# Optimization experiments

Measured on AMD Instinct MI355X. Metric: run time of the kernel, lower is better.

The kernel has to match this reference:

```python
import jax, jax.numpy as jnp
import numpy as np

NUM_WINDOWS = 162   # icosphere order-2 windows
NUM_HEADS = 8

def layernorm(x, g, b, eps=1e-5):
    m = jnp.mean(x, axis=-1, keepdims=True)
    v = jnp.var(x, axis=-1, keepdims=True)
    return (x - m) * jax.lax.rsqrt(v + eps) * g + b

def setup_inputs() -> dict:
    key = jax.random.key(0)
    ks = jax.random.split(key, 16)
    B, N, C = 1, 41472, 512
    H, hid = NUM_HEADS, 4 * 512
    s = 0.02
    # window assignment: 162 windows x 256 vertices, shuffled (gather-based partition)
    rng = np.random.default_rng(0)
    wid = np.repeat(np.arange(NUM_WINDOWS), N // NUM_WINDOWS)
    rng.shuffle(wid)
    return {
        "x": jax.random.normal(ks[0], (B, N, C), jnp.float32),
        "mesh": jax.random.normal(ks[1], (N, 3), jnp.float32),
        "ln1_g": jnp.ones((C,), jnp.float32),
        "ln1_b": jnp.zeros((C,), jnp.float32),
        "qkv_w": jax.random.normal(ks[2], (C, 3 * C), jnp.float32) * s,
        "qkv_b": jnp.zeros((3 * C,), jnp.float32),
        "rel_bias": jax.random.normal(ks[3], (H, 1, 1), jnp.float32) * s,
        "proj_w": jax.random.normal(ks[4], (C, C), jnp.float32) * s,
        "proj_b": jnp.zeros((C,), jnp.float32),
        "ln2_g": jnp.ones((C,), jnp.float32),
        "ln2_b": jnp.zeros((C,), jnp.float32),
        "ffn_w1": jax.random.normal(ks[5], (C, hid), jnp.float32) * s,
        "ffn_b1": jnp.zeros((hid,), jnp.float32),
        "ffn_w2": jax.random.normal(ks[6], (hid, C), jnp.float32) * s,
        "ffn_b2": jnp.zeros((C,), jnp.float32),
        "window_ids": jnp.asarray(wid, dtype=jnp.int32),
    }

def reference(x, mesh, ln1_g, ln1_b, qkv_w, qkv_b, rel_bias, proj_w, proj_b,
              ln2_g, ln2_b, ffn_w1, ffn_b1, ffn_w2, ffn_b2, window_ids):
    B, N, C = x.shape
    H = NUM_HEADS
    hd = C // H
    ws = N // NUM_WINDOWS
    # --- gather-based window partition ---
    idx = jnp.argsort(window_ids)                      # [N]
    w = x[:, idx, :].reshape(B * NUM_WINDOWS, ws, C)   # [BW, ws, C]
    # --- window attention on norm1(windows) ---
    h = layernorm(w, ln1_g, ln1_b)
    qkv = (h @ qkv_w + qkv_b).reshape(B * NUM_WINDOWS, ws, 3, H, hd)
    q, k, v = qkv[:, :, 0], qkv[:, :, 1], qkv[:, :, 2]  # [BW, ws, H, hd]
    scale = hd ** -0.5
    attn = jnp.einsum('wqhd,wkhd->whqk', q, k) * scale + rel_bias
    attn = jax.nn.softmax(attn, axis=-1)
    out = jnp.einsum('whqk,wkhd->wqhd', attn, v).reshape(B * NUM_WINDOWS, ws, C)
    out = out @ proj_w + proj_b
    # --- reverse partition + residual ---
    inv = jnp.argsort(idx)
    x = x + out.reshape(B, N, C)[:, inv, :]
    # --- FFN block ---
    h2 = layernorm(x, ln2_g, ln2_b)
    f = jax.nn.gelu(h2 @ ffn_w1 + ffn_b1, approximate=False) @ ffn_w2 + ffn_b2
    x = x + f
    return (x, mesh)
```

## Files before the change

kernel.cpp:

```cpp
#include <hip/hip_runtime.h>
#include <hip/hip_bf16.h>
#include <math.h>

#define NW   162
#define WS   256
#define NH   8
#define HD   64
#define CC   512
#define NTOK 41472
#define HID  2048

typedef __bf16 bf16x8 __attribute__((ext_vector_type(8)));
typedef float  floatx4 __attribute__((ext_vector_type(4)));

__device__ __forceinline__ void gload_lds16(const __bf16* g, __bf16* l) {
    __builtin_amdgcn_global_load_lds((const __attribute__((address_space(1))) void*)g,
                                     (__attribute__((address_space(3))) void*)l,
                                     16, 0, 0);
}

__global__ __launch_bounds__(256)
void build_perm_atomic(const int* __restrict__ wid, int* __restrict__ perm,
                       int* __restrict__ pos, int* __restrict__ counters) {
    const int i = blockIdx.x * 256 + threadIdx.x;
    const int w = wid[i];
    const int r = atomicAdd(&counters[w], 1);
    perm[w * WS + r] = i;
    pos[i] = w * WS + r;
}

__global__ void transpose_bf16(const float* __restrict__ in,
                               __bf16* __restrict__ out, int K, int N) {
    int idx = blockIdx.x * 256 + threadIdx.x;
    if (idx >= K * N) return;
    int n = idx / K, k = idx - n * K;
    out[idx] = (__bf16)in[(size_t)k * N + n];
}

__global__ __launch_bounds__(64)
void ln1_gather(const float* __restrict__ x, const int* __restrict__ perm,
                const float* __restrict__ g, const float* __restrict__ b,
                __bf16* __restrict__ h) {
    const int j = blockIdx.x, lane = threadIdx.x;
    const int orig = perm[j];
    const float4* xp = (const float4*)(x + (size_t)orig * CC);
    float4 a0 = xp[lane * 2 + 0], a1 = xp[lane * 2 + 1];
    float s  = a0.x + a0.y + a0.z + a0.w + a1.x + a1.y + a1.z + a1.w;
    float sq = a0.x*a0.x + a0.y*a0.y + a0.z*a0.z + a0.w*a0.w
             + a1.x*a1.x + a1.y*a1.y + a1.z*a1.z + a1.w*a1.w;
#pragma unroll
    for (int o = 32; o; o >>= 1) { s += __shfl_xor(s, o); sq += __shfl_xor(sq, o); }
    const float m  = s * (1.f / CC);
    const float rs = rsqrtf(sq * (1.f / CC) - m * m + 1e-5f);
    const float4* g4 = (const float4*)g;  const float4* b4 = (const float4*)b;
    float4 g0 = g4[lane*2+0], g1 = g4[lane*2+1], bb0 = b4[lane*2+0], bb1 = b4[lane*2+1];
    bf16x8 o8;
    o8[0] = (__bf16)((a0.x - m) * rs * g0.x + bb0.x);
    o8[1] = (__bf16)((a0.y - m) * rs * g0.y + bb0.y);
    o8[2] = (__bf16)((a0.z - m) * rs * g0.z + bb0.z);
    o8[3] = (__bf16)((a0.w - m) * rs * g0.w + bb0.w);
    o8[4] = (__bf16)((a1.x - m) * rs * g1.x + bb1.x);
    o8[5] = (__bf16)((a1.y - m) * rs * g1.y + bb1.y);
    o8[6] = (__bf16)((a1.z - m) * rs * g1.z + bb1.z);
    o8[7] = (__bf16)((a1.w - m) * rs * g1.w + bb1.w);
    *(bf16x8*)(h + (size_t)j * CC + lane * 8) = o8;
}

__global__ __launch_bounds__(64)
void resid_ln2(const float* __restrict__ x, const float* __restrict__ ptmp,
               const int* __restrict__ pos, const float* __restrict__ g,
               const float* __restrict__ b, float* __restrict__ xout,
               __bf16* __restrict__ h2) {
    const int i = blockIdx.x, lane = threadIdx.x;
    const int p = pos[i];
    const float4* xp = (const float4*)(x + (size_t)i * CC);
    const float4* pp = (const float4*)(ptmp + (size_t)p * CC);
    float4 a0 = xp[lane*2+0], a1 = xp[lane*2+1];
    float4 t0 = pp[lane*2+0], t1 = pp[lane*2+1];
    a0.x += t0.x; a0.y += t0.y; a0.z += t0.z; a0.w += t0.w;
    a1.x += t1.x; a1.y += t1.y; a1.z += t1.z; a1.w += t1.w;
    float4* op = (float4*)(xout + (size_t)i * CC);
    op[lane*2+0] = a0; op[lane*2+1] = a1;
    float s  = a0.x + a0.y + a0.z + a0.w + a1.x + a1.y + a1.z + a1.w;
    float sq = a0.x*a0.x + a0.y*a0.y + a0.z*a0.z + a0.w*a0.w
             + a1.x*a1.x + a1.y*a1.y + a1.z*a1.z + a1.w*a1.w;
#pragma unroll
    for (int o = 32; o; o >>= 1) { s += __shfl_xor(s, o); sq += __shfl_xor(sq, o); }
    const float m  = s * (1.f / CC);
    const float rs = rsqrtf(sq * (1.f / CC) - m * m + 1e-5f);
    const float4* g4 = (const float4*)g;  const float4* b4 = (const float4*)b;
    float4 g0 = g4[lane*2+0], g1 = g4[lane*2+1], bb0 = b4[lane*2+0], bb1 = b4[lane*2+1];
    bf16x8 o8;
    o8[0] = (__bf16)((a0.x - m) * rs * g0.x + bb0.x);
    o8[1] = (__bf16)((a0.y - m) * rs * g0.y + bb0.y);
    o8[2] = (__bf16)((a0.z - m) * rs * g0.z + bb0.z);
    o8[3] = (__bf16)((a0.w - m) * rs * g0.w + bb0.w);
    o8[4] = (__bf16)((a1.x - m) * rs * g1.x + bb1.x);
    o8[5] = (__bf16)((a1.y - m) * rs * g1.y + bb1.y);
    o8[6] = (__bf16)((a1.z - m) * rs * g1.z + bb1.z);
    o8[7] = (__bf16)((a1.w - m) * rs * g1.w + bb1.w);
    *(bf16x8*)(h2 + (size_t)i * CC + lane * 8) = o8;
}

template <int EPI>
__global__ __launch_bounds__(256)
void gemm_bt(const __bf16* __restrict__ A, const __bf16* __restrict__ Bt,
             const float* __restrict__ bias, const float* __restrict__ res,
             float* __restrict__ Cf, __bf16* __restrict__ Cb,
             int M, int N, int K) {
    __shared__ __bf16 As[128 * 64];
    __shared__ __bf16 Bs[128 * 64];
    const int tid = threadIdx.x;
    const int wave = tid >> 6, lane = tid & 63;
    const int wm = wave & 1, wn = wave >> 1;
    const int bm = blockIdx.y, bn = blockIdx.x;
    const int lr = lane & 15, lq = lane >> 4;

    floatx4 acc[4][4];
#pragma unroll
    for (int i = 0; i < 4; i++)
#pragma unroll
        for (int j = 0; j < 4; j++) acc[i][j] = (floatx4){0.f, 0.f, 0.f, 0.f};

    const int srow = tid >> 3;
    const int sseg = (tid & 7) ^ (srow & 7);
    const __bf16* gA = A  + (size_t)(bm * 128 + srow) * K + sseg * 8;
    const __bf16* gB = Bt + (size_t)(bn * 128 + srow) * K + sseg * 8;
    __bf16* lA = As + (size_t)(wave * 64) * 8;
    __bf16* lB = Bs + (size_t)(wave * 64) * 8;

    for (int kt = 0; kt < K; kt += 64) {
        __syncthreads();
#pragma unroll
        for (int j = 0; j < 4; j++) {
            gload_lds16(gA + (size_t)(j * 32) * K + kt, lA + j * 2048);
            gload_lds16(gB + (size_t)(j * 32) * K + kt, lB + j * 2048);
        }
        __syncthreads();
#pragma unroll
        for (int kk = 0; kk < 2; kk++) {
            bf16x8 af[4], bfr[4];
#pragma unroll
            for (int mt = 0; mt < 4; mt++)
                af[mt] = *(const bf16x8*)(As + (wm * 64 + mt * 16 + lr) * 64 +
                                          (((kk * 4 + lq) ^ (lr & 7)) * 8));
#pragma unroll
            for (int nt = 0; nt < 4; nt++)
                bfr[nt] = *(const bf16x8*)(Bs + (wn * 64 + nt * 16 + lr) * 64 +
                                           (((kk * 4 + lq) ^ (lr & 7)) * 8));
#pragma unroll
            for (int mt = 0; mt < 4; mt++)
#pragma unroll
                for (int nt = 0; nt < 4; nt++)
                    acc[mt][nt] = __builtin_amdgcn_mfma_f32_16x16x32_bf16(
                        af[mt], bfr[nt], acc[mt][nt], 0, 0, 0);
        }
    }

    if constexpr (EPI == 0 || EPI == 2) {
        __syncthreads();
        __bf16* rb = wm ? Bs : As;
#pragma unroll
        for (int mt = 0; mt < 4; mt++)
#pragma unroll
            for (int nt = 0; nt < 4; nt++) {
                const int cl = wn * 64 + nt * 16 + lr;
                const float bv = bias[bn * 128 + cl];
#pragma unroll
                for (int r = 0; r < 4; r++) {
                    float v = acc[mt][nt][r] + bv;
                    if constexpr (EPI == 2) {
                        const float u = 0.79788456080286535588f * (v + 0.044715f * v * v * v);
                        const float t = 1.f - 2.f / (1.f + __expf(2.f * u));
                        v = 0.5f * v * (1.f + t);
                    }
                    rb[(mt * 16 + lq * 4 + r) * 128 + cl] = (__bf16)v;
                }
            }
        __syncthreads();
#pragma unroll
        for (int j = 0; j < 8; j++) {
            const int c = j * 256 + tid;
            const __bf16* reg = (j < 4) ? As : Bs;
            const int rc = c & 1023;
            const int row = rc >> 4, seg = rc & 15;
            bf16x8 val = *(const bf16x8*)(reg + row * 128 + seg * 8);
            *(bf16x8*)(Cb + (size_t)(bm * 128 + (j >> 2) * 64 + row) * N +
                       bn * 128 + seg * 8) = val;
        }
    } else {
#pragma unroll
        for (int mt = 0; mt < 4; mt++) {
            const int row = bm * 128 + wm * 64 + mt * 16 + lq * 4;
#pragma unroll
            for (int nt = 0; nt < 4; nt++) {
                const int col = bn * 128 + wn * 64 + nt * 16 + lr;
                const float bv = bias[col];
#pragma unroll
                for (int r = 0; r < 4; r++) {
                    float v = acc[mt][nt][r] + bv;
                    const size_t off = (size_t)(row + r) * N + col;
                    if constexpr (EPI == 1) Cf[off] = v;
                    else                    Cf[off] = res[off] + v;
                }
            }
        }
    }
}

__global__ __launch_bounds__(256)
void attn_mfma(const __bf16* __restrict__ qkv, __bf16* __restrict__ aout,
               const float* __restrict__ rel_bias) {
    __shared__ __bf16 vs[WS][66];
    __shared__ __bf16 pbuf[4][64][34];
    const int w = blockIdx.x, h = blockIdx.y;
    const int tid = threadIdx.x;
    const int wave = tid >> 6, lane = tid & 63;
    const int lr = lane & 15, lq = lane >> 4;
    const size_t base = (size_t)w * (WS * 1536) + h * 64;

    for (int c = tid; c < WS * 8; c += 256) {
        const int key = c >> 3, d8 = c & 7;
        *(bf16x8*)(&vs[key][d8 * 8]) =
            *(const bf16x8*)(qkv + base + 1024 + (size_t)key * 1536 + d8 * 8);
    }

    const int q0 = wave * 64;
    bf16x8 qf[4][2];
#pragma unroll
    for (int mt = 0; mt < 4; mt++)
#pragma unroll
        for (int kk = 0; kk < 2; kk++)
            qf[mt][kk] = *(const bf16x8*)(qkv + base +
                (size_t)(q0 + mt * 16 + lr) * 1536 + kk * 32 + lq * 8);

    __syncthreads();

    floatx4 o[4][4];
    float lsum[4][4];
#pragma unroll
    for (int mt = 0; mt < 4; mt++)
#pragma unroll
        for (int dt = 0; dt < 4; dt++) o[mt][dt] = (floatx4){0.f, 0.f, 0.f, 0.f};
#pragma unroll
    for (int mt = 0; mt < 4; mt++)
#pragma unroll
        for (int r = 0; r < 4; r++) lsum[mt][r] = 0.f;

    const float sc = 0.125f * 1.44269504089f;
    const float bb = rel_bias[h] * 1.44269504089f;

    for (int kt = 0; kt < 8; kt++) {
        const int kbase = kt * 32;
        floatx4 s[4][2];
#pragma unroll
        for (int mt = 0; mt < 4; mt++)
#pragma unroll
            for (int nt = 0; nt < 2; nt++) s[mt][nt] = (floatx4){0.f, 0.f, 0.f, 0.f};
#pragma unroll
        for (int nt = 0; nt < 2; nt++) {
            const __bf16* kp = qkv + base + 512 + (size_t)(kbase + nt * 16 + lr) * 1536 + lq * 8;
            bf16x8 kf0 = *(const bf16x8*)(kp);
            bf16x8 kf1 = *(const bf16x8*)(kp + 32);
#pragma unroll
            for (int mt = 0; mt < 4; mt++) {
                s[mt][nt] = __builtin_amdgcn_mfma_f32_16x16x32_bf16(qf[mt][0], kf0, s[mt][nt], 0, 0, 0);
                s[mt][nt] = __builtin_amdgcn_mfma_f32_16x16x32_bf16(qf[mt][1], kf1, s[mt][nt], 0, 0, 0);
            }
        }
#pragma unroll
        for (int mt = 0; mt < 4; mt++)
#pragma unroll
            for (int nt = 0; nt < 2; nt++)
#pragma unroll
                for (int r = 0; r < 4; r++) {
                    float e = exp2f(s[mt][nt][r] * sc + bb);
                    lsum[mt][r] += e;
                    pbuf[wave][mt * 16 + lq * 4 + r][nt * 16 + lr] = (__bf16)e;
                }
        __syncthreads();
        bf16x8 vf[4];
#pragma unroll
        for (int dt = 0; dt < 4; dt++)
#pragma unroll
            for (int j = 0; j < 8; j++)
                vf[dt][j] = vs[kbase + lq * 8 + j][dt * 16 + lr];
#pragma unroll
        for (int mt = 0; mt < 4; mt++) {
            bf16x8 pf = *(const bf16x8*)(&pbuf[wave][mt * 16 + lr][lq * 8]);
#pragma unroll
            for (int dt = 0; dt < 4; dt++)
                o[mt][dt] = __builtin_amdgcn_mfma_f32_16x16x32_bf16(pf, vf[dt], o[mt][dt], 0, 0, 0);
        }
        __syncthreads();
    }

#pragma unroll
    for (int mt = 0; mt < 4; mt++)
#pragma unroll
        for (int r = 0; r < 4; r++) {
            float v = lsum[mt][r];
            v += __shfl_xor(v, 1); v += __shfl_xor(v, 2);
            v += __shfl_xor(v, 4); v += __shfl_xor(v, 8);
            lsum[mt][r] = 1.f / v;
        }

#pragma unroll
    for (int dh = 0; dh < 2; dh++) {
#pragma unroll
        for (int mt = 0; mt < 4; mt++)
#pragma unroll
            for (int dt = 0; dt < 2; dt++)
#pragma unroll
                for (int r = 0; r < 4; r++)
                    pbuf[wave][mt * 16 + lq * 4 + r][dt * 16 + lr] =
                        (__bf16)(o[mt][dh * 2 + dt][r] * lsum[mt][r]);
        __syncthreads();
#pragma unroll
        for (int it = 0; it < 4; it++) {
            const int c = it * 64 + lane;
            const int row = c >> 2, seg = c & 3;
            bf16x8 val = *(const bf16x8*)(&pbuf[wave][row][seg * 8]);
            *(bf16x8*)(aout + (size_t)(w * WS + q0 + row) * CC + h * 64 + dh * 32 + seg * 8) = val;
        }
        __syncthreads();
    }
}

extern "C" void kernel_launch(void* const* d_in, const int* in_sizes, int n_in,
                              void* d_out, int out_size, void* d_ws, size_t ws_size,
                              hipStream_t stream) {
    const float* x      = (const float*)d_in[0];
    const float* mesh   = (const float*)d_in[1];
    const float* ln1_g  = (const float*)d_in[2];
    const float* ln1_b  = (const float*)d_in[3];
    const float* qkv_w  = (const float*)d_in[4];
    const float* qkv_b  = (const float*)d_in[5];
    const float* rel_b  = (const float*)d_in[6];
    const float* proj_w = (const float*)d_in[7];
    const float* proj_b = (const float*)d_in[8];
    const float* ln2_g  = (const float*)d_in[9];
    const float* ln2_b  = (const float*)d_in[10];
    const float* w1     = (const float*)d_in[11];
    const float* b1     = (const float*)d_in[12];
    const float* w2     = (const float*)d_in[13];
    const float* b2     = (const float*)d_in[14];
    const int*   wid    = (const int*)d_in[15];

    char* ws = (char*)d_ws;
    int*    perm  = (int*)(ws + 0);
    int*    pos   = (int*)(ws + 165888);
    __bf16* wqkv  = (__bf16*)(ws + 331776);
    __bf16* wproj = (__bf16*)(ws + 1904640);
    __bf16* w1t   = (__bf16*)(ws + 2428928);
    __bf16* w2t   = (__bf16*)(ws + 4526080);
    const size_t BB = 6623232;
    __bf16* hln1 = (__bf16*)(ws + BB);
    __bf16* qkv  = (__bf16*)(ws + BB + 42467328);
    __bf16* aout = (__bf16*)(ws + BB + 169869312);
    float*  ptmp = (float*)(ws + BB);
    __bf16* h2   = (__bf16*)(ws + BB + 84934656);
    __bf16* f1   = (__bf16*)(ws + BB + 127401984);
    float*  xout = (float*)d_out;
    int*    counters = (int*)aout;

    hipMemsetAsync(counters, 0, NW * sizeof(int), stream);
    build_perm_atomic<<<NTOK / 256, 256, 0, stream>>>(wid, perm, pos, counters);

    transpose_bf16<<<(512 * 1536 + 255) / 256, 256, 0, stream>>>(qkv_w, wqkv, 512, 1536);
    transpose_bf16<<<(512 * 512 + 255) / 256, 256, 0, stream>>>(proj_w, wproj, 512, 512);
    transpose_bf16<<<(512 * 2048 + 255) / 256, 256, 0, stream>>>(w1, w1t, 512, 2048);
    transpose_bf16<<<(2048 * 512 + 255) / 256, 256, 0, stream>>>(w2, w2t, 2048, 512);

    ln1_gather<<<NTOK, 64, 0, stream>>>(x, perm, ln1_g, ln1_b, hln1);

    gemm_bt<0><<<dim3(1536 / 128, NTOK / 128), 256, 0, stream>>>(
        hln1, wqkv, qkv_b, nullptr, nullptr, qkv, NTOK, 1536, 512);

    attn_mfma<<<dim3(NW, NH), 256, 0, stream>>>(qkv, aout, rel_b);

    gemm_bt<1><<<dim3(512 / 128, NTOK / 128), 256, 0, stream>>>(
        aout, wproj, proj_b, nullptr, ptmp, nullptr, NTOK, 512, 512);

    resid_ln2<<<NTOK, 64, 0, stream>>>(x, ptmp, pos, ln2_g, ln2_b, xout, h2);

    gemm_bt<2><<<dim3(2048 / 128, NTOK / 128), 256, 0, stream>>>(
        h2, w1t, b1, nullptr, nullptr, f1, NTOK, 2048, 512);

    gemm_bt<3><<<dim3(512 / 128, NTOK / 128), 256, 0, stream>>>(
        f1, w2t, b2, xout, xout, nullptr, NTOK, 512, 2048);

    hipMemcpyAsync((char*)d_out + (size_t)NTOK * CC * 4, mesh,
                   (size_t)NTOK * 3 * 4, hipMemcpyDeviceToDevice, stream);
}
```

Baseline: 834.5 us.

## Swizzle transposed V in LDS, prefetch K, drop barriers, cheaper GELU

In the window attention kernel, V is now stored in LDS transposed with an XOR swizzle, so each lane fetches its MFMA B-fragment with one 16-byte load instead of eight scalar reads. K fragments for the next tile are loaded into registers one step ahead. Block-wide barriers around the per-wave P buffer are removed, since each wave only touches its own slice. The FFN GELU epilogue changes from the tanh form to x*sigmoid(1.702x) with a hardware reciprocal, and the softmax normalisation uses the same fast reciprocal. The sigmoid form and the fast reciprocal add numerical error relative to the exact-erf reference.

Measured after the change: 795.8 us. 4.6% less time.

```diff
diff --git a/kernel.cpp b/kernel.cpp
--- a/kernel.cpp
+++ b/kernel.cpp
@@ -18,6 +18,7 @@
                                      (__attribute__((address_space(3))) void*)l,
                                      16, 0, 0);
 }
+__device__ __forceinline__ float fast_rcp(float x) { return __builtin_amdgcn_rcpf(x); }
 
 __global__ __launch_bounds__(256)
 void build_perm_atomic(const int* __restrict__ wid, int* __restrict__ perm,
@@ -170,9 +171,8 @@
                 for (int r = 0; r < 4; r++) {
                     float v = acc[mt][nt][r] + bv;
                     if constexpr (EPI == 2) {
-                        const float u = 0.79788456080286535588f * (v + 0.044715f * v * v * v);
-                        const float t = 1.f - 2.f / (1.f + __expf(2.f * u));
-                        v = 0.5f * v * (1.f + t);
+                        const float e = __expf(v * -1.702f);
+                        v = v * fast_rcp(1.f + e);
                     }
                     rb[(mt * 16 + lq * 4 + r) * 128 + cl] = (__bf16)v;
                 }
@@ -211,7 +211,7 @@
 __global__ __launch_bounds__(256)
 void attn_mfma(const __bf16* __restrict__ qkv, __bf16* __restrict__ aout,
                const float* __restrict__ rel_bias) {
-    __shared__ __bf16 vs[WS][66];
+    __shared__ __bf16 vsT[HD * WS];
     __shared__ __bf16 pbuf[4][64][34];
     const int w = blockIdx.x, h = blockIdx.y;
     const int tid = threadIdx.x;
@@ -221,8 +221,12 @@
 
     for (int c = tid; c < WS * 8; c += 256) {
         const int key = c >> 3, d8 = c & 7;
-        *(bf16x8*)(&vs[key][d8 * 8]) =
-            *(const bf16x8*)(qkv + base + 1024 + (size_t)key * 1536 + d8 * 8);
+        bf16x8 vv = *(const bf16x8*)(qkv + base + 1024 + (size_t)key * 1536 + d8 * 8);
+#pragma unroll
+        for (int jj = 0; jj < 8; jj++) {
+            const int d = d8 * 8 + jj;
+            vsT[d * WS + (((key >> 3) ^ (d & 31)) << 3) + (key & 7)] = vv[jj];
+        }
     }
 
     const int q0 = wave * 64;
@@ -249,25 +253,39 @@
 
     const float sc = 0.125f * 1.44269504089f;
     const float bb = rel_bias[h] * 1.44269504089f;
+    const __bf16* kp0 = qkv + base + 512;
+
+    bf16x8 kc[2][2];
+#pragma unroll
+    for (int nt = 0; nt < 2; nt++) {
+        const __bf16* kp = kp0 + (size_t)(nt * 16 + lr) * 1536 + lq * 8;
+        kc[nt][0] = *(const bf16x8*)(kp);
+        kc[nt][1] = *(const bf16x8*)(kp + 32);
+    }
 
     for (int kt = 0; kt < 8; kt++) {
         const int kbase = kt * 32;
+        bf16x8 kn[2][2];
+        if (kt < 7) {
+#pragma unroll
+            for (int nt = 0; nt < 2; nt++) {
+                const __bf16* kp = kp0 + (size_t)(kbase + 32 + nt * 16 + lr) * 1536 + lq * 8;
+                kn[nt][0] = *(const bf16x8*)(kp);
+                kn[nt][1] = *(const bf16x8*)(kp + 32);
+            }
+        }
         floatx4 s[4][2];
 #pragma unroll
         for (int mt = 0; mt < 4; mt++)
 #pragma unroll
             for (int nt = 0; nt < 2; nt++) s[mt][nt] = (floatx4){0.f, 0.f, 0.f, 0.f};
 #pragma unroll
-        for (int nt = 0; nt < 2; nt++) {
-            const __bf16* kp = qkv + base + 512 + (size_t)(kbase + nt * 16 + lr) * 1536 + lq * 8;
-            bf16x8 kf0 = *(const bf16x8*)(kp);
-            bf16x8 kf1 = *(const bf16x8*)(kp + 32);
+        for (int nt = 0; nt < 2; nt++)
 #pragma unroll
             for (int mt = 0; mt < 4; mt++) {
-                s[mt][nt] = __builtin_amdgcn_mfma_f32_16x16x32_bf16(qf[mt][0], kf0, s[mt][nt], 0, 0, 0);
-                s[mt][nt] = __builtin_amdgcn_mfma_f32_16x16x32_bf16(qf[mt][1], kf1, s[mt][nt], 0, 0, 0);
+                s[mt][nt] = __builtin_amdgcn_mfma_f32_16x16x32_bf16(qf[mt][0], kc[nt][0], s[mt][nt], 0, 0, 0);
+                s[mt][nt] = __builtin_amdgcn_mfma_f32_16x16x32_bf16(qf[mt][1], kc[nt][1], s[mt][nt], 0, 0, 0);
             }
-        }
 #pragma unroll
         for (int mt = 0; mt < 4; mt++)
 #pragma unroll
@@ -278,13 +296,13 @@
                     lsum[mt][r] += e;
                     pbuf[wave][mt * 16 + lq * 4 + r][nt * 16 + lr] = (__bf16)e;
                 }
-        __syncthreads();
         bf16x8 vf[4];
 #pragma unroll
-        for (int dt = 0; dt < 4; dt++)
-#pragma unroll
-            for (int j = 0; j < 8; j++)
-                vf[dt][j] = vs[kbase + lq * 8 + j][dt * 16 + lr];
+        for (int dt = 0; dt < 4; dt++) {
+            const int d = dt * 16 + lr;
+            vf[dt] = *(const bf16x8*)(vsT + d * WS +
+                                      (((kt * 4 + lq) ^ (d & 31)) << 3));
+        }
 #pragma unroll
         for (int mt = 0; mt < 4; mt++) {
             bf16x8 pf = *(const bf16x8*)(&pbuf[wave][mt * 16 + lr][lq * 8]);
@@ -292,7 +310,8 @@
             for (int dt = 0; dt < 4; dt++)
                 o[mt][dt] = __builtin_amdgcn_mfma_f32_16x16x32_bf16(pf, vf[dt], o[mt][dt], 0, 0, 0);
         }
-        __syncthreads();
+#pragma unroll
+        for (int nt = 0; nt < 2; nt++) { kc[nt][0] = kn[nt][0]; kc[nt][1] = kn[nt][1]; }
     }
 
 #pragma unroll
@@ -302,7 +321,7 @@
             float v = lsum[mt][r];
             v += __shfl_xor(v, 1); v += __shfl_xor(v, 2);
             v += __shfl_xor(v, 4); v += __shfl_xor(v, 8);
-            lsum[mt][r] = 1.f / v;
+            lsum[mt][r] = fast_rcp(v);
         }
 
 #pragma unroll
@@ -315,7 +334,6 @@
                 for (int r = 0; r < 4; r++)
                     pbuf[wave][mt * 16 + lq * 4 + r][dt * 16 + lr] =
                         (__bf16)(o[mt][dh * 2 + dt][r] * lsum[mt][r]);
-        __syncthreads();
 #pragma unroll
         for (int it = 0; it < 4; it++) {
             const int c = it * 64 + lane;
@@ -323,7 +341,6 @@
             bf16x8 val = *(const bf16x8*)(&pbuf[wave][row][seg * 8]);
             *(bf16x8*)(aout + (size_t)(w * WS + q0 + row) * CC + h * 64 + dh * 32 + seg * 8) = val;
         }
-        __syncthreads();
     }
 }
 
```
